# Performance work log

Hardware: AMD Instinct MI355X
Metric: run time of the kernel (lower is better)

Reference implementation:

```python
import jax, jax.numpy as jnp
import numpy as np

D = 64  # query_dimensions (power of 2, required by Hadamard)
N, L, H = 8, 8192, 8


def fwht(x):
    """Unnormalized fast Walsh-Hadamard transform along the last axis.
    x: (..., d), d a power of 2."""
    orig_shape = x.shape
    d = orig_shape[-1]
    x = x.reshape(-1, d)
    h = 1
    while h < d:  # log2(d) stages, static under jit
        x = x.reshape(-1, d // (2 * h), 2, h)
        a, b = x[:, :, 0, :], x[:, :, 1, :]
        x = jnp.stack([a + b, a - b], axis=2).reshape(-1, d)
        h *= 2
    return x.reshape(orig_shape)


def setup_inputs() -> dict:
    key = jax.random.key(0)
    kx, kb, kg, ks, kp = jax.random.split(key, 5)
    x = jax.random.normal(kx, (N, L, H, D), dtype=jnp.float32)
    # B: random signs in {-1, +1}
    B = jnp.where(jax.random.bernoulli(kb, 0.5, (D,)), 1.0, -1.0).astype(jnp.float32)
    # G: standard normal
    G = jax.random.normal(kg, (D,), dtype=jnp.float32)
    # S: chi(df=D) samples, divided by ||G|| (as in new_feature_map)
    chi_samples = jnp.linalg.norm(jax.random.normal(ks, (D, D), dtype=jnp.float32), axis=1)
    S = chi_samples / jnp.linalg.norm(G)
    # P: random permutation of [0, D)
    P = jax.random.permutation(kp, D).astype(jnp.int32)
    return {"x": x, "B": B, "G": G, "S": S, "P": P}


def reference(x, B, G, S, P):
    # softmax_temp defaults to 1/sqrt(query_dimensions)
    softmax_temp = 1.0 / np.sqrt(D)
    x_shape = x.shape
    y = (x * np.sqrt(softmax_temp)).reshape(-1, D)
    y = fwht(y * B)          # H B x
    y = y[:, P] * G          # G P H B x
    y = fwht(y) * S          # S H G P H B x
    return (np.sqrt(1.0 / D) * y).reshape(x_shape)
```

## Files before the change

### kernel.cpp

```cpp
#include <hip/hip_runtime.h>


typedef float f32x4 __attribute__((ext_vector_type(4)));

#define FSTAGE(H)                                                   \
    _Pragma("unroll")                                               \
    for (int i = 0; i < 64; i += 2*(H)) {                           \
        _Pragma("unroll")                                           \
        for (int j = 0; j < (H); ++j) {                             \
            const float a = y[i+j], b = y[i+j+(H)];                 \
            y[i+j] = a + b; y[i+j+(H)] = a - b;                     \
        }                                                           \
    }

__global__ __launch_bounds__(128) void fastfood_kernel(
    const float* __restrict__ x,
    const float* __restrict__ Bv,
    const float* __restrict__ Gv,
    const float* __restrict__ Sv,
    const int*   __restrict__ Pv,
    float* __restrict__ out,
    int ntiles)
{
    __shared__ float lds_all[2 * 64 * 64];
    const int l  = threadIdx.x & 63;
    const int wv = threadIdx.x >> 6;
    float* lds = &lds_all[wv * 4096];

    const int wid    = blockIdx.x * 2 + wv;
    const int nwaves = gridDim.x * 2;

    const int hi = l >> 4;
    const int lo = l & 15;
    const int e0 = lo << 2;
    const int swl = lo << 2;

    const float c1 = 0.35355339059327373f;
    const float c2 = 0.125f;

    const float bs0 = Bv[e0+0]*c1, bs1 = Bv[e0+1]*c1, bs2 = Bv[e0+2]*c1, bs3 = Bv[e0+3]*c1;
    const float gg0 = Gv[e0+0],    gg1 = Gv[e0+1],    gg2 = Gv[e0+2],    gg3 = Gv[e0+3];
    const float ss0 = Sv[e0+0]*c2, ss1 = Sv[e0+1]*c2, ss2 = Sv[e0+2]*c2, ss3 = Sv[e0+3]*c2;
    const int   p0  = Pv[e0+0],    p1  = Pv[e0+1],    p2  = Pv[e0+2],    p3  = Pv[e0+3];

    const f32x4* __restrict__ xin  = (const f32x4*)x;
    f32x4* __restrict__       yout = (f32x4*)out;

    int t = wid;
    if (t >= ntiles) return;

    f32x4 st[16];
    {
        const long long tb = (long long)t * 1024;
        #pragma unroll
        for (int c = 0; c < 16; ++c) st[c] = xin[tb + c*64 + l];
    }

    for (; t < ntiles; t += nwaves) {
        const long long tb = (long long)t * 1024;

        #pragma unroll
        for (int c = 0; c < 16; ++c) {
            const int r = 4*c + hi;
            f32x4 v = st[c];
            v.x *= bs0; v.y *= bs1; v.z *= bs2; v.w *= bs3;
            *(f32x4*)&lds[r*64 + (e0 ^ ((r & 15) << 2))] = v;
        }

        float y[64];
        #pragma unroll
        for (int k = 0; k < 16; ++k) {
            const f32x4 v = *(const f32x4*)&lds[l*64 + ((k << 2) ^ swl)];
            y[4*k+0] = v.x; y[4*k+1] = v.y; y[4*k+2] = v.z; y[4*k+3] = v.w;
        }

        FSTAGE(1) FSTAGE(2) FSTAGE(4) FSTAGE(8) FSTAGE(16) FSTAGE(32)

        #pragma unroll
        for (int k = 0; k < 16; ++k) {
            f32x4 v;
            v.x = y[4*k+0]; v.y = y[4*k+1]; v.z = y[4*k+2]; v.w = y[4*k+3];
            *(f32x4*)&lds[l*64 + ((k << 2) ^ swl)] = v;
        }

        #pragma unroll
        for (int c = 0; c < 16; ++c) {
            const int r  = 4*c + hi;
            const int rb = r * 64;
            const int sw = (r & 15) << 2;
            const float a0 = lds[rb + (p0 ^ sw)];
            const float a1 = lds[rb + (p1 ^ sw)];
            const float a2 = lds[rb + (p2 ^ sw)];
            const float a3 = lds[rb + (p3 ^ sw)];
            f32x4 v;
            v.x = a0 * gg0; v.y = a1 * gg1; v.z = a2 * gg2; v.w = a3 * gg3;
            *(f32x4*)&lds[rb + (e0 ^ sw)] = v;
        }

        {
            const long long tn = (t + nwaves < ntiles) ? (long long)(t + nwaves)
                                                       : (long long)t;
            const long long nb = tn * 1024;
            #pragma unroll
            for (int c = 0; c < 16; ++c) st[c] = xin[nb + c*64 + l];
        }

        #pragma unroll
        for (int k = 0; k < 16; ++k) {
            const f32x4 v = *(const f32x4*)&lds[l*64 + ((k << 2) ^ swl)];
            y[4*k+0] = v.x; y[4*k+1] = v.y; y[4*k+2] = v.z; y[4*k+3] = v.w;
        }

        FSTAGE(1) FSTAGE(2) FSTAGE(4) FSTAGE(8) FSTAGE(16) FSTAGE(32)

        #pragma unroll
        for (int k = 0; k < 16; ++k) {
            f32x4 v;
            v.x = y[4*k+0]; v.y = y[4*k+1]; v.z = y[4*k+2]; v.w = y[4*k+3];
            *(f32x4*)&lds[l*64 + ((k << 2) ^ swl)] = v;
        }

        #pragma unroll
        for (int c = 0; c < 16; ++c) {
            const int r = 4*c + hi;
            f32x4 v = *(const f32x4*)&lds[r*64 + (e0 ^ ((r & 15) << 2))];
            v.x *= ss0; v.y *= ss1; v.z *= ss2; v.w *= ss3;
            __builtin_nontemporal_store(v, &yout[tb + c*64 + l]);
        }
    }
}

extern "C" void kernel_launch(void* const* d_in, const int* in_sizes, int n_in,
                              void* d_out, int out_size, void* d_ws, size_t ws_size,
                              hipStream_t stream) {
    const float* x = (const float*)d_in[0];
    const float* B = (const float*)d_in[1];
    const float* G = (const float*)d_in[2];
    const float* S = (const float*)d_in[3];
    const int*   P = (const int*)d_in[4];
    float* out = (float*)d_out;

    const int ntiles = in_sizes[0] / 4096;

    const int block = 128;
    const int grid  = 1280;
    fastfood_kernel<<<grid, block, 0, stream>>>(x, B, G, S, P, out, ntiles);
}
```

Before: 52.95 us.

## Split each 64-wide row FWHT across two lanes using permlane32 swap

```diff
diff --git a/kernel.cpp b/kernel.cpp
--- a/kernel.cpp
+++ b/kernel.cpp
@@ -2,10 +2,17 @@
 
 
 typedef float f32x4 __attribute__((ext_vector_type(4)));
+typedef unsigned u32x2 __attribute__((ext_vector_type(2)));
 
-#define FSTAGE(H)                                                   \
+__device__ __forceinline__ float partner32(float v, bool hh) {
+    const unsigned u = __float_as_uint(v);
+    const u32x2 r = __builtin_amdgcn_permlane32_swap(u, u, false, false);
+    return __uint_as_float(hh ? r.x : r.y);
+}
+
+#define FSTAGE32(H)                                                 \
     _Pragma("unroll")                                               \
-    for (int i = 0; i < 64; i += 2*(H)) {                           \
+    for (int i = 0; i < 32; i += 2*(H)) {                           \
         _Pragma("unroll")                                           \
         for (int j = 0; j < (H); ++j) {                             \
             const float a = y[i+j], b = y[i+j+(H)];                 \
@@ -13,7 +20,7 @@
         }                                                           \
     }
 
-__global__ __launch_bounds__(128) void fastfood_kernel(
+__global__ __launch_bounds__(128, 5) void fastfood_kernel(
     const float* __restrict__ x,
     const float* __restrict__ Bv,
     const float* __restrict__ Gv,
@@ -22,10 +29,10 @@
     float* __restrict__ out,
     int ntiles)
 {
-    __shared__ float lds_all[2 * 64 * 64];
+    __shared__ float lds_all[2 * 2048];
     const int l  = threadIdx.x & 63;
     const int wv = threadIdx.x >> 6;
-    float* lds = &lds_all[wv * 4096];
+    float* lds = &lds_all[wv * 2048];
 
     const int wid    = blockIdx.x * 2 + wv;
     const int nwaves = gridDim.x * 2;
@@ -33,7 +40,10 @@
     const int hi = l >> 4;
     const int lo = l & 15;
     const int e0 = lo << 2;
-    const int swl = lo << 2;
+    const int rr = l & 31;
+    const bool hh = (l >= 32);
+    const int cb = hh ? 32 : 0;
+    const int swzr = (rr & 15) << 2;
 
     const float c1 = 0.35355339059327373f;
     const float c2 = 0.125f;
@@ -49,42 +59,47 @@
     int t = wid;
     if (t >= ntiles) return;
 
-    f32x4 st[16];
+    f32x4 st[8];
     {
-        const long long tb = (long long)t * 1024;
+        const long long tb = (long long)t * 512;
         #pragma unroll
-        for (int c = 0; c < 16; ++c) st[c] = xin[tb + c*64 + l];
+        for (int c = 0; c < 8; ++c) st[c] = xin[tb + c*64 + l];
     }
 
     for (; t < ntiles; t += nwaves) {
-        const long long tb = (long long)t * 1024;
+        const long long tb = (long long)t * 512;
 
         #pragma unroll
-        for (int c = 0; c < 16; ++c) {
+        for (int c = 0; c < 8; ++c) {
             const int r = 4*c + hi;
             f32x4 v = st[c];
             v.x *= bs0; v.y *= bs1; v.z *= bs2; v.w *= bs3;
             *(f32x4*)&lds[r*64 + (e0 ^ ((r & 15) << 2))] = v;
         }
 
-        float y[64];
+        float y[32];
         #pragma unroll
-        for (int k = 0; k < 16; ++k) {
-            const f32x4 v = *(const f32x4*)&lds[l*64 + ((k << 2) ^ swl)];
+        for (int k = 0; k < 8; ++k) {
+            const f32x4 v = *(const f32x4*)&lds[rr*64 + ((cb + 4*k) ^ swzr)];
             y[4*k+0] = v.x; y[4*k+1] = v.y; y[4*k+2] = v.z; y[4*k+3] = v.w;
         }
 
-        FSTAGE(1) FSTAGE(2) FSTAGE(4) FSTAGE(8) FSTAGE(16) FSTAGE(32)
-
+        FSTAGE32(1) FSTAGE32(2) FSTAGE32(4) FSTAGE32(8) FSTAGE32(16)
         #pragma unroll
-        for (int k = 0; k < 16; ++k) {
-            f32x4 v;
-            v.x = y[4*k+0]; v.y = y[4*k+1]; v.z = y[4*k+2]; v.w = y[4*k+3];
-            *(f32x4*)&lds[l*64 + ((k << 2) ^ swl)] = v;
+        for (int i = 0; i < 32; ++i) {
+            const float opp = partner32(y[i], hh);
+            y[i] = hh ? (opp - y[i]) : (y[i] + opp);
         }
 
         #pragma unroll
-        for (int c = 0; c < 16; ++c) {
+        for (int k = 0; k < 8; ++k) {
+            f32x4 v;
+            v.x = y[4*k+0]; v.y = y[4*k+1]; v.z = y[4*k+2]; v.w = y[4*k+3];
+            *(f32x4*)&lds[rr*64 + ((cb + 4*k) ^ swzr)] = v;
+        }
+
+        #pragma unroll
+        for (int c = 0; c < 8; ++c) {
             const int r  = 4*c + hi;
             const int rb = r * 64;
             const int sw = (r & 15) << 2;
@@ -97,31 +112,34 @@
             *(f32x4*)&lds[rb + (e0 ^ sw)] = v;
         }
 
-        {
-            const long long tn = (t + nwaves < ntiles) ? (long long)(t + nwaves)
-                                                       : (long long)t;
-            const long long nb = tn * 1024;
+        if (t + nwaves < ntiles) {
+            const long long nb = (long long)(t + nwaves) * 512;
             #pragma unroll
-            for (int c = 0; c < 16; ++c) st[c] = xin[nb + c*64 + l];
+            for (int c = 0; c < 8; ++c) st[c] = xin[nb + c*64 + l];
         }
 
         #pragma unroll
-        for (int k = 0; k < 16; ++k) {
-            const f32x4 v = *(const f32x4*)&lds[l*64 + ((k << 2) ^ swl)];
+        for (int k = 0; k < 8; ++k) {
+            const f32x4 v = *(const f32x4*)&lds[rr*64 + ((cb + 4*k) ^ swzr)];
             y[4*k+0] = v.x; y[4*k+1] = v.y; y[4*k+2] = v.z; y[4*k+3] = v.w;
         }
 
-        FSTAGE(1) FSTAGE(2) FSTAGE(4) FSTAGE(8) FSTAGE(16) FSTAGE(32)
-
+        FSTAGE32(1) FSTAGE32(2) FSTAGE32(4) FSTAGE32(8) FSTAGE32(16)
         #pragma unroll
-        for (int k = 0; k < 16; ++k) {
-            f32x4 v;
-            v.x = y[4*k+0]; v.y = y[4*k+1]; v.z = y[4*k+2]; v.w = y[4*k+3];
-            *(f32x4*)&lds[l*64 + ((k << 2) ^ swl)] = v;
+        for (int i = 0; i < 32; ++i) {
+            const float opp = partner32(y[i], hh);
+            y[i] = hh ? (opp - y[i]) : (y[i] + opp);
         }
 
         #pragma unroll
-        for (int c = 0; c < 16; ++c) {
+        for (int k = 0; k < 8; ++k) {
+            f32x4 v;
+            v.x = y[4*k+0]; v.y = y[4*k+1]; v.z = y[4*k+2]; v.w = y[4*k+3];
+            *(f32x4*)&lds[rr*64 + ((cb + 4*k) ^ swzr)] = v;
+        }
+
+        #pragma unroll
+        for (int c = 0; c < 8; ++c) {
             const int r = 4*c + hi;
             f32x4 v = *(const f32x4*)&lds[r*64 + (e0 ^ ((r & 15) << 2))];
             v.x *= ss0; v.y *= ss1; v.z *= ss2; v.w *= ss3;
@@ -140,9 +158,9 @@
     const int*   P = (const int*)d_in[4];
     float* out = (float*)d_out;
 
-    const int ntiles = in_sizes[0] / 4096;
+    const int ntiles = in_sizes[0] / 2048;
 
     const int block = 128;
-    const int grid  = 1280;
+    const int grid  = 2560;
     fastfood_kernel<<<grid, block, 0, stream>>>(x, B, G, S, P, out, ntiles);
 }
```

Measured after the change: 158.4 us. 2.99x slower.
